# Kernel optimization log

Hardware: AMD Instinct MI355X
Metric: run time of the kernel (lower is better)

The kernel has to match this reference:

```python
import jax, jax.numpy as jnp
import numpy as np
import math

C_S, C_Z = 384, 128
N_HEAD, C = 12, 16
N_QP, N_PV = 4, 8
B, N_RES = 1, 384


def quat_to_rot(q):
    # q: (..., 4) unnormalized quaternion -> (..., 3, 3) rotation matrix
    q = q / jnp.linalg.norm(q, axis=-1, keepdims=True)
    w, x, y, z = q[..., 0], q[..., 1], q[..., 2], q[..., 3]
    R = jnp.stack([
        1 - 2 * (y * y + z * z), 2 * (x * y - w * z), 2 * (x * z + w * y),
        2 * (x * y + w * z), 1 - 2 * (x * x + z * z), 2 * (y * z - w * x),
        2 * (x * z - w * y), 2 * (y * z + w * x), 1 - 2 * (x * x + y * y),
    ], axis=-1)
    return R.reshape(q.shape[:-1] + (3, 3))


def warp_3d_point(T, p):
    # T: (..., 1, 1, N, 4, 4) rigid transforms; p: (..., H, P, N, 3)
    R = T[..., :3, :3]
    t = T[..., :3, 3]
    return jnp.squeeze(R @ p[..., None], -1) + t


def warp_3d_point_inv(T, p):
    # Inverse rigid transform: R^T (p - t)
    R = T[..., :3, :3]
    t = T[..., :3, 3]
    return jnp.squeeze(jnp.swapaxes(R, -1, -2) @ (p - t)[..., None], -1)


def setup_inputs() -> dict:
    key = jax.random.key(0)
    ks = jax.random.split(key, 24)
    s = jax.random.normal(ks[0], (B, N_RES, C_S), dtype=jnp.float32)
    z = jax.random.normal(ks[1], (B, N_RES, N_RES, C_Z), dtype=jnp.float32)
    # Build rigid backbone transforms T (rotation from random quaternion + translation)
    quat = jax.random.normal(ks[2], (B, N_RES, 4), dtype=jnp.float32)
    trans = jax.random.normal(ks[3], (B, N_RES, 3), dtype=jnp.float32) * 10.0
    R = quat_to_rot(quat)
    T = jnp.zeros((B, N_RES, 4, 4), dtype=jnp.float32)
    T = T.at[..., :3, :3].set(R)
    T = T.at[..., :3, 3].set(trans)
    T = T.at[..., 3, 3].set(1.0)

    def lin(k, din, dout):
        kw, kb = jax.random.split(k)
        W = jax.random.normal(kw, (din, dout), dtype=jnp.float32) * 0.02
        b = jax.random.normal(kb, (dout,), dtype=jnp.float32) * 0.01
        return W, b

    Wq, bq = lin(ks[4], C_S, N_HEAD * C)
    Wk, bk = lin(ks[5], C_S, N_HEAD * C)
    Wv, bv = lin(ks[6], C_S, N_HEAD * C)
    Wqp, bqp = lin(ks[7], C_S, 3 * N_QP * N_HEAD)
    Wkp, bkp = lin(ks[8], C_S, 3 * N_QP * N_HEAD)
    Wvp, bvp = lin(ks[9], C_S, 3 * N_PV * N_HEAD)
    Wb, bb = lin(ks[10], C_Z, N_HEAD)
    d_out_in = N_HEAD * C_Z + N_HEAD * C + N_HEAD * 4 * N_PV
    Wo, bo = lin(ks[11], d_out_in, C_S)
    head_weights = jax.random.normal(ks[12], (N_HEAD,), dtype=jnp.float32) * 0.1
    return dict(s=s, z=z, T=T, Wq=Wq, bq=bq, Wk=Wk, bk=bk, Wv=Wv, bv=bv,
                Wqp=Wqp, bqp=bqp, Wkp=Wkp, bkp=bkp, Wvp=Wvp, bvp=bvp,
                Wb=Wb, bb=bb, Wo=Wo, bo=bo, head_weights=head_weights)


def ipa_forward(s, z, T, Wq, bq, Wk, bk, Wv, bv, Wqp, bqp, Wkp, bkp,
                Wvp, bvp, Wb, bb, Wo, bo, head_weights):
    batch = s.shape[:-2]
    n = s.shape[-2]
    # --- prepare qkv ---
    def heads(x):  # (..., N, H*C) -> (..., H, N, C)
        return jnp.moveaxis(x.reshape(batch + (n, N_HEAD, C)), -3, -2)
    q = heads(s @ Wq + bq)
    k = heads(s @ Wk + bk)
    v = heads(s @ Wv + bv)

    def pts(x, P):  # (..., N, 3*H*P) -> (..., H, P, N, 3)
        x = x.reshape(batch + (n, 3, N_HEAD, P))
        return jnp.moveaxis(x, (-4, -3), (-2, -1))
    qp = pts(s @ Wqp + bqp, N_QP)
    kp = pts(s @ Wkp + bkp, N_QP)
    vp = pts(s @ Wvp + bvp, N_PV)

    # --- attention scores (Alg 22 line 7) ---
    wc = math.sqrt(2.0 / (9.0 * N_QP))
    wl = math.sqrt(1.0 / 3.0)
    gamma = jax.nn.softplus(head_weights).reshape(-1, 1, 1)  # (H,1,1)
    q = q * (1.0 / math.sqrt(C))
    bias = jnp.moveaxis(z @ Wb + bb, -1, -3)  # (..., H, N, N)
    qk = jnp.einsum('...hic,...hjc->...hij', q, k)
    T_bc = T.reshape(batch + (1, 1, n, 4, 4))
    tqp = warp_3d_point(T_bc, qp)[..., :, None, :]   # (..., H, QP, N, 1, 3)
    tkp = warp_3d_point(T_bc, kp)[..., None, :, :]   # (..., H, QP, 1, N, 3)
    sq_dist = jnp.sum((tqp - tkp) ** 2, axis=-1)      # (..., H, QP, N, N)
    qpkp_term = gamma * (wc / 2.0) * jnp.sum(sq_dist, axis=-3)  # (..., H, N, N)
    att = jax.nn.softmax(wl * (qk + bias - qpkp_term), axis=-1)

    # --- outputs ---
    pairwise = jnp.einsum('...ijc,...hij->...hic', z, att)
    pairwise = jnp.moveaxis(pairwise, -3, -2).reshape(batch + (n, N_HEAD * C_Z))
    v_out = jnp.einsum('...hij,...hjc->...hic', att, v)
    v_out = jnp.moveaxis(v_out, -3, -2).reshape(batch + (n, N_HEAD * C))
    vt = warp_3d_point(T_bc, vp)                                # (..., H, PV, N, 3)
    v_att = jnp.einsum('...hij,...hkjp->...hkip', att, vt)     # (..., H, PV, N, 3)
    v_tr = warp_3d_point_inv(T_bc, v_att)                       # (..., H, PV, N, 3)
    v_tr = jnp.einsum('...hpic->...ichp', v_tr)                 # (..., N, 3, H, PV)
    norm = jnp.linalg.norm(v_tr, axis=-3, keepdims=True)        # (..., N, 1, H, PV)
    vp_norm = norm.reshape(batch + (n, N_HEAD * N_PV))
    vp_out = v_tr.reshape(batch + (n, 3 * N_HEAD * N_PV))

    out = jnp.concatenate([v_out, vp_out, vp_norm, pairwise], axis=-1)
    return out @ Wo + bo


def reference(s, z, T, Wq, bq, Wk, bk, Wv, bv, Wqp, bqp, Wkp, bkp,
              Wvp, bvp, Wb, bb, Wo, bo, head_weights):
    return ipa_forward(s, z, T, Wq, bq, Wk, bk, Wv, bv, Wqp, bqp, Wkp, bkp,
                       Wvp, bvp, Wb, bb, Wo, bo, head_weights)
```

## Files before the change

### kernel.cpp

```cpp
#include <hip/hip_runtime.h>
#include <math.h>

#define NRES 384
#define NH   12
#define WLc 0.5773502691896258f
#define WCc 0.23570226039551587f

typedef __attribute__((ext_vector_type(8))) _Float16 half8;
typedef __attribute__((ext_vector_type(4))) float f32x4;

#define OFF_P    0
#define OFF_SH   442368
#define OFF_WCT  516096
#define OFF_BCT  737280
#define OFF_QE   738432
#define OFF_KE   885888
#define OFF_VET  1033344
#define OFF_WOT  1143936
#define OFF_CAT  1549440
#define OFF_ATT  1954944
#define OFF_BIAS 2839680
#define OFF_Z16  3724416

__global__ __launch_bounds__(256) void pack_bias(
    const float* __restrict__ s,  const float* __restrict__ z,
    const float* __restrict__ Wq,  const float* __restrict__ bq,
    const float* __restrict__ Wk,  const float* __restrict__ bk,
    const float* __restrict__ Wv,  const float* __restrict__ bv,
    const float* __restrict__ Wqp, const float* __restrict__ bqp,
    const float* __restrict__ Wkp, const float* __restrict__ bkp,
    const float* __restrict__ Wvp, const float* __restrict__ bvp,
    const float* __restrict__ Wb,  const float* __restrict__ bb,
    const float* __restrict__ Wo,
    float* __restrict__ ws)
{
    int b = blockIdx.x, t = threadIdx.x;
    __shared__ float tile[64 * 65];
    __shared__ _Float16 wbT[16 * 136];
    __shared__ float sbb[16];
    __shared__ _Float16 zL[64 * 136];

    if (b >= 451) {
        _Float16* biasb = (_Float16*)(ws + OFF_BIAS);
        _Float16* z16t  = (_Float16*)(ws + OFF_Z16);
        int bi = b - 451;
        size_t m0 = (size_t)bi * 64;
        int ib = bi / 6, j0 = (bi % 6) * 64;
        if (t < 128) {
            #pragma unroll
            for (int h = 0; h < 12; h++) wbT[h * 136 + t] = (_Float16)(WLc * Wb[t * 12 + h]);
            #pragma unroll
            for (int h = 12; h < 16; h++) wbT[h * 136 + t] = (_Float16)0.f;
        }
        if (t < 16) sbb[t] = (t < 12) ? WLc * bb[t] : 0.f;
        __syncthreads();
        int w = t >> 6, lane = t & 63;
        int m = lane & 15, q = lane >> 4;
        size_t ri = m0 + w * 16 + m;
        const float* zr = z + ri * 128 + q * 8;
        f32x4 acc = {0};
        #pragma unroll
        for (int sI = 0; sI < 4; sI++) {
            float4 v0 = *(const float4*)(zr + sI * 32);
            float4 v1 = *(const float4*)(zr + sI * 32 + 4);
            half8 a;
            a[0]=(_Float16)v0.x; a[1]=(_Float16)v0.y; a[2]=(_Float16)v0.z; a[3]=(_Float16)v0.w;
            a[4]=(_Float16)v1.x; a[5]=(_Float16)v1.y; a[6]=(_Float16)v1.z; a[7]=(_Float16)v1.w;
            *(half8*)(zL + (w * 16 + m) * 136 + sI * 32 + q * 8) = a;
            half8 bf = *(const half8*)(wbT + m * 136 + sI * 32 + q * 8);
            acc = __builtin_amdgcn_mfma_f32_16x16x32_f16(a, bf, acc, 0, 0, 0);
        }
        __syncthreads();
        {
            int c = t & 127, jh = t >> 7;
            _Float16 vals[32];
            #pragma unroll
            for (int u = 0; u < 32; u++) vals[u] = zL[(jh * 32 + u) * 136 + c];
            _Float16* dst = z16t + ((size_t)ib * 128 + c) * 384 + j0 + jh * 32;
            #pragma unroll
            for (int g = 0; g < 4; g++) {
                half8 r;
                #pragma unroll
                for (int u = 0; u < 8; u++) r[u] = vals[g * 8 + u];
                *(half8*)(dst + g * 8) = r;
            }
        }
        if (m < 12) {
            #pragma unroll
            for (int r = 0; r < 4; r++)
                biasb[(size_t)m * 147456 + m0 + w * 16 + q * 4 + r] = (_Float16)(acc[r] + sbb[m]);
        }
        return;
    }

    _Float16* sh  = (_Float16*)(ws + OFF_SH);
    _Float16* wct = (_Float16*)(ws + OFF_WCT);
    _Float16* wot = (_Float16*)(ws + OFF_WOT);
    float* bct = ws + OFF_BCT;

    if (b < 144) {
        int id = b * 256 + t;
        float4 v = ((const float4*)s)[id];
        _Float16 r[4] = { (_Float16)v.x, (_Float16)v.y, (_Float16)v.z, (_Float16)v.w };
        *(uint2*)(sh + id * 4) = *(uint2*)r;
        return;
    }
    if (b < 252) {
        int ti = b - 144;
        int k0 = (ti % 6) * 64, n0 = (ti / 6) * 64;
        int cl = t & 63, rg = t >> 6;
        int ncat = n0 + cl;
        const float* W; int dout, col;
        if      (ncat < 192) { W = Wq;  dout = 192; col = ncat; }
        else if (ncat < 384) { W = Wk;  dout = 192; col = ncat - 192; }
        else if (ncat < 576) { W = Wv;  dout = 192; col = ncat - 384; }
        else if (ncat < 720) { W = Wqp; dout = 144; col = ncat - 576; }
        else if (ncat < 864) { W = Wkp; dout = 144; col = ncat - 720; }
        else                 { W = Wvp; dout = 288; col = ncat - 864; }
        #pragma unroll
        for (int u = 0; u < 16; u++) {
            int r = rg * 16 + u;
            tile[r * 65 + cl] = W[(size_t)(k0 + r) * dout + col];
        }
        __syncthreads();
        #pragma unroll
        for (int u2 = 0; u2 < 2; u2++) {
            int item = t + 256 * u2;
            int nl = item >> 3, kg = item & 7;
            half8 rr;
            #pragma unroll
            for (int jj = 0; jj < 8; jj++) rr[jj] = (_Float16)tile[(kg * 8 + jj) * 65 + nl];
            *(half8*)(wct + (size_t)(n0 + nl) * 384 + k0 + kg * 8) = rr;
        }
        return;
    }
    if (b < 450) {
        int ti = b - 252;
        int k0 = (ti % 33) * 64, n0 = (ti / 33) * 64;
        int cl = t & 63, rg = t >> 6;
        #pragma unroll
        for (int u = 0; u < 16; u++) {
            int r = rg * 16 + u;
            tile[r * 65 + cl] = Wo[(size_t)(k0 + r) * 384 + n0 + cl];
        }
        __syncthreads();
        #pragma unroll
        for (int u2 = 0; u2 < 2; u2++) {
            int item = t + 256 * u2;
            int nl = item >> 3, kg = item & 7;
            half8 rr;
            #pragma unroll
            for (int jj = 0; jj < 8; jj++) rr[jj] = (_Float16)tile[(kg * 8 + jj) * 65 + nl];
            *(half8*)(wot + (size_t)(n0 + nl) * 2112 + k0 + kg * 8) = rr;
        }
        return;
    }
    for (int e = t; e < 1152; e += 256) {
        float bv_;
        if      (e < 192) bv_ = bq[e];
        else if (e < 384) bv_ = bk[e - 192];
        else if (e < 576) bv_ = bv[e - 384];
        else if (e < 720) bv_ = bqp[e - 576];
        else if (e < 864) bv_ = bkp[e - 720];
        else              bv_ = bvp[e - 864];
        bct[e] = bv_;
    }
}

__global__ __launch_bounds__(256) void proj_mfma(float* __restrict__ ws)
{
    const _Float16* sh  = (const _Float16*)(ws + OFF_SH);
    const _Float16* wct = (const _Float16*)(ws + OFF_WCT);
    const float* bct = ws + OFF_BCT;
    float* P = ws + OFF_P;

    __shared__ float sAcc[2][16][65];

    int t = threadIdx.x, w = t >> 6, lane = t & 63;
    int m = lane & 15, q = lane >> 4;
    int mh = w & 1, kh = w >> 1;
    int n0 = blockIdx.x * 64, m0 = blockIdx.y * 32 + mh * 16;

    f32x4 acc[4] = {0};
    const _Float16* arow = sh + (size_t)(m0 + m) * 384 + kh * 192;
    #pragma unroll 3
    for (int s = 0; s < 6; s++) {
        int k = s * 32 + q * 8;
        half8 a = *(const half8*)(arow + k);
        #pragma unroll
        for (int nt = 0; nt < 4; nt++) {
            half8 b = *(const half8*)(wct + (size_t)(n0 + nt * 16 + m) * 384 + kh * 192 + k);
            acc[nt] = __builtin_amdgcn_mfma_f32_16x16x32_f16(a, b, acc[nt], 0, 0, 0);
        }
    }
    if (kh == 0) {
        #pragma unroll
        for (int nt = 0; nt < 4; nt++)
            #pragma unroll
            for (int r = 0; r < 4; r++)
                sAcc[mh][q * 4 + r][nt * 16 + m] = acc[nt][r];
    }
    __syncthreads();
    if (kh == 1) {
        #pragma unroll
        for (int nt = 0; nt < 4; nt++) {
            int col = n0 + nt * 16 + m;
            float bias = bct[col];
            #pragma unroll
            for (int r = 0; r < 4; r++)
                P[(size_t)(m0 + q * 4 + r) * 1152 + col] =
                    acc[nt][r] + sAcc[mh][q * 4 + r][nt * 16 + m] + bias;
        }
    }
}

__global__ __launch_bounds__(192) void prep_kernel(
    const float* __restrict__ T, const float* __restrict__ hw,
    float* __restrict__ ws)
{
    int i = blockIdx.x, t = threadIdx.x;
    const float* pr = ws + OFF_P + (size_t)i * 1152;
    float* Qe = ws + OFF_QE;
    float* Ke = ws + OFF_KE;
    _Float16* vet = (_Float16*)(ws + OFF_VET);

    __shared__ float sT[16], sG[12];
    __shared__ float sTQ[12][4][3], sTK[12][4][3];
    if (t < 16) sT[t] = T[i * 16 + t];
    if (t < 12) { float x = hw[t]; sG[t] = (x > 20.f) ? x : log1pf(__expf(x)); }
    __syncthreads();
    float R00=sT[0],R01=sT[1],R02=sT[2],t0=sT[3];
    float R10=sT[4],R11=sT[5],R12=sT[6],t1=sT[7];
    float R20=sT[8],R21=sT[9],R22=sT[10],t2=sT[11];

    if (t < 48) {
        int h = t >> 2, p = t & 3;
        float a0 = pr[576 + 0*48 + h*4 + p], a1 = pr[576 + 1*48 + h*4 + p], a2 = pr[576 + 2*48 + h*4 + p];
        sTQ[h][p][0] = R00*a0 + R01*a1 + R02*a2 + t0;
        sTQ[h][p][1] = R10*a0 + R11*a1 + R12*a2 + t1;
        sTQ[h][p][2] = R20*a0 + R21*a1 + R22*a2 + t2;
    } else if (t < 96) {
        int tt = t - 48, h = tt >> 2, p = tt & 3;
        float a0 = pr[720 + 0*48 + h*4 + p], a1 = pr[720 + 1*48 + h*4 + p], a2 = pr[720 + 2*48 + h*4 + p];
        sTK[h][p][0] = R00*a0 + R01*a1 + R02*a2 + t0;
        sTK[h][p][1] = R10*a0 + R11*a1 + R12*a2 + t1;
        sTK[h][p][2] = R20*a0 + R21*a1 + R22*a2 + t2;
    } else {
        int tt = t - 96, h = tt >> 3, p = tt & 7;
        float a0 = pr[864 + 0*96 + h*8 + p], a1 = pr[864 + 1*96 + h*8 + p], a2 = pr[864 + 2*96 + h*8 + p];
        vet[(size_t)(h*48 + 16 + p*3 + 0) * 384 + i] = (_Float16)(R00*a0 + R01*a1 + R02*a2 + t0);
        vet[(size_t)(h*48 + 16 + p*3 + 1) * 384 + i] = (_Float16)(R10*a0 + R11*a1 + R12*a2 + t1);
        vet[(size_t)(h*48 + 16 + p*3 + 2) * 384 + i] = (_Float16)(R20*a0 + R21*a1 + R22*a2 + t2);
    }
    {
        int h = t >> 4, c = t & 15;
        vet[(size_t)(h*48 + c) * 384 + i] = (_Float16)pr[384 + h*16 + c];
        if (t < 96) vet[(size_t)((t>>3)*48 + 40 + (t&7)) * 384 + i] = (_Float16)0.f;
        Qe[(size_t)i*384 + h*32 + c] = WLc * 0.25f * pr[h*16 + c];
        Ke[((size_t)h*384 + i)*32 + c] = pr[192 + h*16 + c];
    }
    __syncthreads();
    if (t < 144) {
        int h = t / 12, d = t % 12, p = d / 3, r = d % 3;
        float gw = WLc * sG[h] * WCc;
        Qe[(size_t)i*384 + h*32 + 16 + d] = gw * sTQ[h][p][r];
        Ke[((size_t)h*384 + i)*32 + 16 + d] = sTK[h][p][r];
    }
    if (t < 12) {
        int h = t;
        float sqq = 0.f, sqk = 0.f;
        #pragma unroll
        for (int p = 0; p < 4; p++)
            #pragma unroll
            for (int r = 0; r < 3; r++) { sqq += sTQ[h][p][r]*sTQ[h][p][r]; sqk += sTK[h][p][r]*sTK[h][p][r]; }
        float gw = WLc * sG[h] * WCc;
        Qe[(size_t)i*384 + h*32 + 28] = -0.5f * gw;
        Qe[(size_t)i*384 + h*32 + 29] = -0.5f * gw * sqq;
        Qe[(size_t)i*384 + h*32 + 30] = 0.f;
        Qe[(size_t)i*384 + h*32 + 31] = 0.f;
        Ke[((size_t)h*384 + i)*32 + 28] = sqk;
        Ke[((size_t)h*384 + i)*32 + 29] = 1.f;
        Ke[((size_t)h*384 + i)*32 + 30] = 0.f;
        Ke[((size_t)h*384 + i)*32 + 31] = 0.f;
    }
}

__global__ __launch_bounds__(512) void logits_out40(
    const float* __restrict__ T, float* __restrict__ ws)
{
    __shared__ float sQe[8 * 32];
    __shared__ float sLg[8][384];
    __shared__ float sMS[16];
    __shared__ _Float16 sAttL[8 * 392];
    __shared__ float sO[8 * 49];
    __shared__ float sT8[8 * 16];

    int h = blockIdx.y, i0 = blockIdx.x * 8;
    int t = threadIdx.x;
    const float* Qe = ws + OFF_QE;
    const float* Ke = ws + OFF_KE;
    const _Float16* biasb = (const _Float16*)(ws + OFF_BIAS);
    const _Float16* vet = (const _Float16*)(ws + OFF_VET);
    _Float16* attg = (_Float16*)(ws + OFF_ATT);
    _Float16* catb = (_Float16*)(ws + OFF_CAT);

    if (t < 256)
        sQe[t] = Qe[(size_t)(i0 + (t >> 5)) * 384 + h * 32 + (t & 31)];
    if (t < 128)
        sT8[t] = T[(size_t)(i0 + (t >> 4)) * 16 + (t & 15)];
    __syncthreads();

    float lgv[8];
    if (t < 384) {
        int j = t;
        float ke[32];
        const float4* kr = (const float4*)(Ke + ((size_t)h * 384 + j) * 32);
        #pragma unroll
        for (int u = 0; u < 8; u++) { float4 v = kr[u]; ke[u*4]=v.x; ke[u*4+1]=v.y; ke[u*4+2]=v.z; ke[u*4+3]=v.w; }
        #pragma unroll
        for (int ii = 0; ii < 8; ii++) {
            float acc = (float)biasb[(size_t)h * 147456 + (size_t)(i0 + ii) * 384 + j];
            #pragma unroll
            for (int c = 0; c < 32; c++) acc += sQe[ii * 32 + c] * ke[c];
            lgv[ii] = acc;
            sLg[ii][j] = acc;
        }
    }
    __syncthreads();
    {
        int w = t >> 6, lane = t & 63;
        float vv[6], mx = -1e30f;
        #pragma unroll
        for (int u = 0; u < 6; u++) { vv[u] = sLg[w][lane + 64 * u]; mx = fmaxf(mx, vv[u]); }
        #pragma unroll
        for (int off = 1; off < 64; off <<= 1) mx = fmaxf(mx, __shfl_xor(mx, off));
        float sm = 0.f;
        #pragma unroll
        for (int u = 0; u < 6; u++) sm += __expf(vv[u] - mx);
        #pragma unroll
        for (int off = 1; off < 64; off <<= 1) sm += __shfl_xor(sm, off);
        if (lane == 0) { sMS[w] = mx; sMS[8 + w] = sm; }
    }
    __syncthreads();
    if (t < 384) {
        int j = t;
        #pragma unroll
        for (int ii = 0; ii < 8; ii++) {
            float a = __expf(lgv[ii] - sMS[ii]) * (1.0f / sMS[8 + ii]);
            attg[((size_t)h * 384 + i0 + ii) * 384 + j] = (_Float16)a;
            sAttL[ii * 392 + j] = (_Float16)a;
        }
    }
    __syncthreads();

    int w = t >> 6, lane = t & 63;
    int m16 = lane & 15, q = lane >> 4;
    if (w < 3) {
        int nt = w;
        f32x4 acc = {0};
        #pragma unroll 3
        for (int s = 0; s < 12; s++) {
            int k = s * 32 + q * 8;
            half8 a;
            if (m16 < 8) a = *(const half8*)(sAttL + m16 * 392 + k);
            else         a = (half8){0,0,0,0,0,0,0,0};
            half8 bfr = *(const half8*)(vet + (size_t)(h * 48 + nt * 16 + m16) * 384 + k);
            acc = __builtin_amdgcn_mfma_f32_16x16x32_f16(a, bfr, acc, 0, 0, 0);
        }
        #pragma unroll
        for (int r = 0; r < 4; r++) {
            int row = q * 4 + r;
            if (row < 8) sO[row * 49 + nt * 16 + m16] = acc[r];
        }
    }
    __syncthreads();

    if (t < 128) {
        int il = t >> 4, c = t & 15;
        catb[(size_t)(i0 + il) * 2112 + h * 16 + c] = (_Float16)sO[il * 49 + c];
    }
    if (t < 64) {
        int il = t >> 3, p = t & 7;
        const float* o = sO + il * 49 + 16 + p * 3;
        const float* Ti = sT8 + il * 16;
        float x0 = o[0] - Ti[3], x1 = o[1] - Ti[7], x2 = o[2] - Ti[11];
        float r0 = Ti[0]*x0 + Ti[4]*x1 + Ti[8]*x2;
        float r1 = Ti[1]*x0 + Ti[5]*x1 + Ti[9]*x2;
        float r2 = Ti[2]*x0 + Ti[6]*x1 + Ti[10]*x2;
        _Float16* cr = catb + (size_t)(i0 + il) * 2112;
        cr[192 + 0*96 + h*8 + p] = (_Float16)r0;
        cr[192 + 1*96 + h*8 + p] = (_Float16)r1;
        cr[192 + 2*96 + h*8 + p] = (_Float16)r2;
        cr[480 + h*8 + p] = (_Float16)sqrtf(r0*r0 + r1*r1 + r2*r2);
    }
}

__global__ __launch_bounds__(256) void pairwise_mfma(float* __restrict__ ws)
{
    __shared__ __attribute__((aligned(16))) _Float16 sPW[1536];
    int i = blockIdx.x;
    int t = threadIdx.x, w = t >> 6, lane = t & 63;
    int m16 = lane & 15, q = lane >> 4;
    const _Float16* attg = (const _Float16*)(ws + OFF_ATT);
    const _Float16* z16t = (const _Float16*)(ws + OFF_Z16);
    _Float16* catb = (_Float16*)(ws + OFF_CAT);

    f32x4 acc0 = {0}, acc1 = {0};
    const _Float16* arow  = attg + ((size_t)(m16 < 12 ? m16 : 0) * 384 + i) * 384;
    const _Float16* zrow0 = z16t + ((size_t)i * 128 + w * 32 + m16) * 384;
    const _Float16* zrow1 = zrow0 + 16 * 384;
    #pragma unroll 4
    for (int ks = 0; ks < 12; ks++) {
        int k = ks * 32 + q * 8;
        half8 a;
        if (m16 < 12) a = *(const half8*)(arow + k);
        else          a = (half8){0,0,0,0,0,0,0,0};
        half8 b0 = *(const half8*)(zrow0 + k);
        half8 b1 = *(const half8*)(zrow1 + k);
        acc0 = __builtin_amdgcn_mfma_f32_16x16x32_f16(a, b0, acc0, 0, 0, 0);
        acc1 = __builtin_amdgcn_mfma_f32_16x16x32_f16(a, b1, acc1, 0, 0, 0);
    }
    if (q < 3) {
        #pragma unroll
        for (int r = 0; r < 4; r++) {
            int h = q * 4 + r;
            sPW[h * 128 + w * 32 + m16]      = (_Float16)acc0[r];
            sPW[h * 128 + w * 32 + 16 + m16] = (_Float16)acc1[r];
        }
    }
    __syncthreads();
    if (t < 192)
        *(half8*)(catb + (size_t)i * 2112 + 576 + t * 8) = *(const half8*)(sPW + t * 8);
}

__global__ __launch_bounds__(256) void outgemm_mfma(
    float* __restrict__ ws, const float* __restrict__ bo, float* __restrict__ out)
{
    const _Float16* catb = (const _Float16*)(ws + OFF_CAT);
    const _Float16* wot = (const _Float16*)(ws + OFF_WOT);

    __shared__ float sAcc[2][16][65];

    int t = threadIdx.x, w = t >> 6, lane = t & 63;
    int m = lane & 15, q = lane >> 4;
    int mh = w & 1, kh = w >> 1;
    int n0 = blockIdx.x * 64;
    int m0 = blockIdx.y * 32 + mh * 16;

    f32x4 acc[4] = {0};
    int row = m0 + m;
    const _Float16* ar = catb + (size_t)row * 2112 + kh * 1056;
    #pragma unroll 3
    for (int s = 0; s < 33; s++) {
        int k = s * 32 + q * 8;
        half8 a = *(const half8*)(ar + k);
        #pragma unroll
        for (int nt = 0; nt < 4; nt++) {
            half8 b = *(const half8*)(wot + (size_t)(n0 + nt * 16 + m) * 2112 + kh * 1056 + k);
            acc[nt] = __builtin_amdgcn_mfma_f32_16x16x32_f16(a, b, acc[nt], 0, 0, 0);
        }
    }
    if (kh == 0) {
        #pragma unroll
        for (int nt = 0; nt < 4; nt++)
            #pragma unroll
            for (int r = 0; r < 4; r++)
                sAcc[mh][q * 4 + r][nt * 16 + m] = acc[nt][r];
    }
    __syncthreads();
    if (kh == 1) {
        #pragma unroll
        for (int nt = 0; nt < 4; nt++) {
            int col = n0 + nt * 16 + m;
            float bv = bo[col];
            #pragma unroll
            for (int r = 0; r < 4; r++)
                out[(size_t)(m0 + q * 4 + r) * 384 + col] =
                    acc[nt][r] + sAcc[mh][q * 4 + r][nt * 16 + m] + bv;
        }
    }
}

extern "C" void kernel_launch(void* const* d_in, const int* in_sizes, int n_in,
                              void* d_out, int out_size, void* d_ws, size_t ws_size,
                              hipStream_t stream)
{
    const float* s   = (const float*)d_in[0];
    const float* z   = (const float*)d_in[1];
    const float* T   = (const float*)d_in[2];
    const float* Wq  = (const float*)d_in[3];
    const float* bq  = (const float*)d_in[4];
    const float* Wk  = (const float*)d_in[5];
    const float* bk  = (const float*)d_in[6];
    const float* Wv  = (const float*)d_in[7];
    const float* bv  = (const float*)d_in[8];
    const float* Wqp = (const float*)d_in[9];
    const float* bqp = (const float*)d_in[10];
    const float* Wkp = (const float*)d_in[11];
    const float* bkp = (const float*)d_in[12];
    const float* Wvp = (const float*)d_in[13];
    const float* bvp = (const float*)d_in[14];
    const float* Wb  = (const float*)d_in[15];
    const float* bb  = (const float*)d_in[16];
    const float* Wo  = (const float*)d_in[17];
    const float* bo  = (const float*)d_in[18];
    const float* hw  = (const float*)d_in[19];
    float* ws  = (float*)d_ws;
    float* out = (float*)d_out;

    pack_bias<<<2755, 256, 0, stream>>>(s, z, Wq, bq, Wk, bk, Wv, bv,
                                        Wqp, bqp, Wkp, bkp, Wvp, bvp, Wb, bb, Wo, ws);
    proj_mfma<<<dim3(18, 12), 256, 0, stream>>>(ws);
    prep_kernel<<<384, 192, 0, stream>>>(T, hw, ws);
    logits_out40<<<dim3(48, 12), 512, 0, stream>>>(T, ws);
    pairwise_mfma<<<384, 256, 0, stream>>>(ws);
    outgemm_mfma<<<dim3(6, 12), 256, 0, stream>>>(ws, bo, out);
}
```

Measured before the change: 223.7 us.

## Split pairwise and output GEMM along K with atomic accumulation

The pairwise kernel now splits the j reduction into three chunks across a new grid dimension and accumulates fp32 partials into a zeroed workspace buffer with atomics. The output GEMM is likewise split three ways along K, reading the pairwise part directly from the fp32 buffer and atomically adding into an output pre-initialised with the bias in prep_kernel. This targets low occupancy in the two tail kernels (72 output blocks, 384 pairwise blocks) at the cost of atomic traffic, extra zeroing and a non-deterministic summation order. The pairwise buffer reuses the projection workspace region at offset zero, which relies on it being dead by then.

```diff
diff --git a/kernel.cpp b/kernel.cpp
--- a/kernel.cpp
+++ b/kernel.cpp
@@ -10,6 +10,7 @@
 typedef __attribute__((ext_vector_type(4))) float f32x4;
 
 #define OFF_P    0
+#define OFF_PW   0
 #define OFF_SH   442368
 #define OFF_WCT  516096
 #define OFF_BCT  737280
@@ -216,6 +217,7 @@
 
 __global__ __launch_bounds__(192) void prep_kernel(
     const float* __restrict__ T, const float* __restrict__ hw,
+    const float* __restrict__ bo, float* __restrict__ out,
     float* __restrict__ ws)
 {
     int i = blockIdx.x, t = threadIdx.x;
@@ -223,6 +225,9 @@
     float* Qe = ws + OFF_QE;
     float* Ke = ws + OFF_KE;
     _Float16* vet = (_Float16*)(ws + OFF_VET);
+
+    out[(size_t)i * 384 + t]       = bo[t];
+    out[(size_t)i * 384 + 192 + t] = bo[192 + t];
 
     __shared__ float sT[16], sG[12];
     __shared__ float sTQ[12][4][3], sTK[12][4][3];
@@ -304,6 +309,11 @@
     _Float16* attg = (_Float16*)(ws + OFF_ATT);
     _Float16* catb = (_Float16*)(ws + OFF_CAT);
 
+    {
+        int bid = blockIdx.y * 48 + blockIdx.x;
+        if (t < 256)
+            ((float4*)(ws + OFF_PW))[bid * 256 + t] = (float4){0.f, 0.f, 0.f, 0.f};
+    }
     if (t < 256)
         sQe[t] = Qe[(size_t)(i0 + (t >> 5)) * 384 + h * 32 + (t & 31)];
     if (t < 128)
@@ -377,7 +387,7 @@
 
     if (t < 128) {
         int il = t >> 4, c = t & 15;
-        catb[(size_t)(i0 + il) * 2112 + h * 16 + c] = (_Float16)sO[il * 49 + c];
+        catb[(size_t)(i0 + il) * 576 + h * 16 + c] = (_Float16)sO[il * 49 + c];
     }
     if (t < 64) {
         int il = t >> 3, p = t & 7;
@@ -387,7 +397,7 @@
         float r0 = Ti[0]*x0 + Ti[4]*x1 + Ti[8]*x2;
         float r1 = Ti[1]*x0 + Ti[5]*x1 + Ti[9]*x2;
         float r2 = Ti[2]*x0 + Ti[6]*x1 + Ti[10]*x2;
-        _Float16* cr = catb + (size_t)(i0 + il) * 2112;
+        _Float16* cr = catb + (size_t)(i0 + il) * 576;
         cr[192 + 0*96 + h*8 + p] = (_Float16)r0;
         cr[192 + 1*96 + h*8 + p] = (_Float16)r1;
         cr[192 + 2*96 + h*8 + p] = (_Float16)r2;
@@ -397,20 +407,19 @@
 
 __global__ __launch_bounds__(256) void pairwise_mfma(float* __restrict__ ws)
 {
-    __shared__ __attribute__((aligned(16))) _Float16 sPW[1536];
-    int i = blockIdx.x;
+    int i = blockIdx.x, jc = blockIdx.y;
     int t = threadIdx.x, w = t >> 6, lane = t & 63;
     int m16 = lane & 15, q = lane >> 4;
     const _Float16* attg = (const _Float16*)(ws + OFF_ATT);
     const _Float16* z16t = (const _Float16*)(ws + OFF_Z16);
-    _Float16* catb = (_Float16*)(ws + OFF_CAT);
+    float* PW = ws + OFF_PW;
 
     f32x4 acc0 = {0}, acc1 = {0};
-    const _Float16* arow  = attg + ((size_t)(m16 < 12 ? m16 : 0) * 384 + i) * 384;
-    const _Float16* zrow0 = z16t + ((size_t)i * 128 + w * 32 + m16) * 384;
+    const _Float16* arow  = attg + ((size_t)(m16 < 12 ? m16 : 0) * 384 + i) * 384 + jc * 128;
+    const _Float16* zrow0 = z16t + ((size_t)i * 128 + w * 32 + m16) * 384 + jc * 128;
     const _Float16* zrow1 = zrow0 + 16 * 384;
-    #pragma unroll 4
-    for (int ks = 0; ks < 12; ks++) {
+    #pragma unroll
+    for (int ks = 0; ks < 4; ks++) {
         int k = ks * 32 + q * 8;
         half8 a;
         if (m16 < 12) a = *(const half8*)(arow + k);
@@ -424,19 +433,17 @@
         #pragma unroll
         for (int r = 0; r < 4; r++) {
             int h = q * 4 + r;
-            sPW[h * 128 + w * 32 + m16]      = (_Float16)acc0[r];
-            sPW[h * 128 + w * 32 + 16 + m16] = (_Float16)acc1[r];
-        }
-    }
-    __syncthreads();
-    if (t < 192)
-        *(half8*)(catb + (size_t)i * 2112 + 576 + t * 8) = *(const half8*)(sPW + t * 8);
+            atomicAdd(&PW[(size_t)i * 1536 + h * 128 + w * 32 + m16],      acc0[r]);
+            atomicAdd(&PW[(size_t)i * 1536 + h * 128 + w * 32 + 16 + m16], acc1[r]);
+        }
+    }
 }
 
 __global__ __launch_bounds__(256) void outgemm_mfma(
-    float* __restrict__ ws, const float* __restrict__ bo, float* __restrict__ out)
+    float* __restrict__ ws, float* __restrict__ out)
 {
     const _Float16* catb = (const _Float16*)(ws + OFF_CAT);
+    const float* PW = ws + OFF_PW;
     const _Float16* wot = (const _Float16*)(ws + OFF_WOT);
 
     __shared__ float sAcc[2][16][65];
@@ -446,17 +453,27 @@
     int mh = w & 1, kh = w >> 1;
     int n0 = blockIdx.x * 64;
     int m0 = blockIdx.y * 32 + mh * 16;
+    int kbase = blockIdx.z * 704 + kh * 352;
 
     f32x4 acc[4] = {0};
     int row = m0 + m;
-    const _Float16* ar = catb + (size_t)row * 2112 + kh * 1056;
-    #pragma unroll 3
-    for (int s = 0; s < 33; s++) {
-        int k = s * 32 + q * 8;
-        half8 a = *(const half8*)(ar + k);
+    #pragma unroll 2
+    for (int s = 0; s < 11; s++) {
+        int kb = kbase + s * 32;
+        int k = kb + q * 8;
+        half8 a;
+        if (kb < 576) {
+            a = *(const half8*)(catb + (size_t)row * 576 + k);
+        } else {
+            const float* pwp = PW + (size_t)row * 1536 + (k - 576);
+            float4 u0 = ((const float4*)pwp)[0];
+            float4 u1 = ((const float4*)pwp)[1];
+            a[0]=(_Float16)u0.x; a[1]=(_Float16)u0.y; a[2]=(_Float16)u0.z; a[3]=(_Float16)u0.w;
+            a[4]=(_Float16)u1.x; a[5]=(_Float16)u1.y; a[6]=(_Float16)u1.z; a[7]=(_Float16)u1.w;
+        }
         #pragma unroll
         for (int nt = 0; nt < 4; nt++) {
-            half8 b = *(const half8*)(wot + (size_t)(n0 + nt * 16 + m) * 2112 + kh * 1056 + k);
+            half8 b = *(const half8*)(wot + (size_t)(n0 + nt * 16 + m) * 2112 + k);
             acc[nt] = __builtin_amdgcn_mfma_f32_16x16x32_f16(a, b, acc[nt], 0, 0, 0);
         }
     }
@@ -472,11 +489,10 @@
         #pragma unroll
         for (int nt = 0; nt < 4; nt++) {
             int col = n0 + nt * 16 + m;
-            float bv = bo[col];
             #pragma unroll
             for (int r = 0; r < 4; r++)
-                out[(size_t)(m0 + q * 4 + r) * 384 + col] =
-                    acc[nt][r] + sAcc[mh][q * 4 + r][nt * 16 + m] + bv;
+                atomicAdd(&out[(size_t)(m0 + q * 4 + r) * 384 + col],
+                          acc[nt][r] + sAcc[mh][q * 4 + r][nt * 16 + m]);
         }
     }
 }
@@ -511,8 +527,8 @@
     pack_bias<<<2755, 256, 0, stream>>>(s, z, Wq, bq, Wk, bk, Wv, bv,
                                         Wqp, bqp, Wkp, bkp, Wvp, bvp, Wb, bb, Wo, ws);
     proj_mfma<<<dim3(18, 12), 256, 0, stream>>>(ws);
-    prep_kernel<<<384, 192, 0, stream>>>(T, hw, ws);
+    prep_kernel<<<384, 192, 0, stream>>>(T, hw, bo, out, ws);
     logits_out40<<<dim3(48, 12), 512, 0, stream>>>(T, ws);
-    pairwise_mfma<<<384, 256, 0, stream>>>(ws);
-    outgemm_mfma<<<dim3(6, 12), 256, 0, stream>>>(ws, bo, out);
-}
+    pairwise_mfma<<<dim3(384, 3), 256, 0, stream>>>(ws);
+    outgemm_mfma<<<dim3(6, 12, 3), 256, 0, stream>>>(ws, out);
+}
```

Result: faster. 216.8 us (-3.1%).
